# Optimization experiments

Measured on AMD Instinct MI355X. Metric: run time of the kernel, lower is better.

The kernel has to match this reference:

```python
import jax, jax.numpy as jnp
import numpy as np

N = 50000
E = 800000
IN_DIM, HID, OUT, DW = 128, 96, 40, 64
N_LBL = 10


def _deg_inv_sqrt(dst, n):
    # PyG gcn_norm: degree over target nodes of (A + I)
    deg = jax.ops.segment_sum(jnp.ones((dst.shape[0],), jnp.float32), dst, num_segments=n) + 1.0
    return jnp.where(deg > 0, 1.0 / jnp.sqrt(deg), 0.0)


def gcn_conv(h_in, W, b, src, dst, dinv):
    # GCNConv: out = D^-1/2 (A + I) D^-1/2 (X W) + b
    h = h_in @ W                                  # [N, F]
    norm = (dinv[src] * dinv[dst])[:, None]       # [E, 1]
    agg = jax.ops.segment_sum(h[src] * norm, dst, num_segments=h.shape[0])
    agg = agg + h * (dinv * dinv)[:, None]        # self-loop term
    return agg + b


def setup_inputs() -> dict:
    key = jax.random.key(0)
    ks = jax.random.split(key, 12)
    inp = {
        "x": jax.random.normal(ks[0], (N, IN_DIM), jnp.float32),
        "y": jax.random.uniform(ks[1], (N, OUT), jnp.float32),
        "edge_index": jax.random.randint(ks[2], (2, E), 0, N, jnp.int64 if jax.config.read("jax_enable_x64") else jnp.int32),
        "deep_walk_emb": jax.random.normal(ks[3], (N, DW), jnp.float32),
        # learned params
        "W_gcn1": jax.random.normal(ks[4], (IN_DIM, HID), jnp.float32) * (1.0 / np.sqrt(IN_DIM)),
        "b_gcn1": jnp.zeros((HID,), jnp.float32),
        "W_gcn2": jax.random.normal(ks[5], (HID, HID), jnp.float32) * (1.0 / np.sqrt(HID)),
        "b_gcn2": jnp.zeros((HID,), jnp.float32),
        "W_lbl": jax.random.normal(ks[6], (N_LBL, OUT, OUT), jnp.float32) * (1.0 / np.sqrt(OUT)),
        "b_lbl": jnp.zeros((N_LBL, OUT), jnp.float32),
        "W_fuse": jax.random.normal(ks[7], (HID + OUT + DW, OUT), jnp.float32) * (1.0 / np.sqrt(HID + OUT + DW)),
        "b_fuse": jnp.zeros((OUT,), jnp.float32),
    }
    return inp


def reference(x, y, edge_index, deep_walk_emb,
              W_gcn1, b_gcn1, W_gcn2, b_gcn2,
              W_lbl, b_lbl, W_fuse, b_fuse):
    src, dst = edge_index[0], edge_index[1]
    dinv = _deg_inv_sqrt(dst, x.shape[0])

    # feature propagation: 2 stacked GCNConv layers
    h = gcn_conv(x, W_gcn1, b_gcn1, src, dst, dinv)
    h = gcn_conv(h, W_gcn2, b_gcn2, src, dst, dinv)

    # label propagation: 10 stacked GCNConv layers via scan over stacked weights
    def step(carry, wb):
        W, b = wb
        return gcn_conv(carry, W, b, src, dst, dinv), None

    x_label, _ = jax.lax.scan(step, y, (W_lbl, b_lbl))

    fused = jnp.concatenate([h, x_label, deep_walk_emb], axis=1)  # [N, HID+OUT+DW]
    out = fused @ W_fuse + b_fuse
    return jax.nn.sigmoid(out)
```

## Files before the change

kernel.cpp:

```cpp
#include <hip/hip_runtime.h>
#include <hip/hip_bf16.h>
#include <math.h>

#define THREADS 256
typedef _Float16 h16;

__device__ __forceinline__ void ld8h(const h16* p, float* f) {
    union { uint4 u; h16 h[8]; } c;
    c.u = *(const uint4*)p;
#pragma unroll
    for (int j = 0; j < 8; ++j) f[j] = (float)c.h[j];
}

__global__ __launch_bounds__(256) void count_part_kernel(
    const int* __restrict__ dst, int* __restrict__ cnt, int E, int n)
{
    const int cls = blockIdx.x & 7;
    const int nb  = gridDim.x >> 3;
    const int sub = blockIdx.x >> 3;
    const int lo = (int)((long long)n * cls / 8);
    const int hi = (int)((long long)n * (cls + 1) / 8);
    const int stride = nb * 256;
    for (int e = sub * 256 + threadIdx.x; e < E; e += stride) {
        int d = dst[e];
        if (d >= lo && d < hi) atomicAdd(&cnt[d], 1);
    }
}

__global__ __launch_bounds__(256) void scatter_part_kernel(
    const int* __restrict__ src, const int* __restrict__ dst,
    int* __restrict__ cursor, int* __restrict__ col, int E, int n)
{
    const int cls = blockIdx.x & 7;
    const int nb  = gridDim.x >> 3;
    const int sub = blockIdx.x >> 3;
    const int lo = (int)((long long)n * cls / 8);
    const int hi = (int)((long long)n * (cls + 1) / 8);
    const int stride = nb * 256;
    for (int e = sub * 256 + threadIdx.x; e < E; e += stride) {
        int d = dst[e];
        if (d >= lo && d < hi) {
            int p = atomicAdd(&cursor[d], 1);
            col[p] = src[e];
        }
    }
}

__global__ __launch_bounds__(256) void scanp1_pre_kernel(
    const int* __restrict__ cnt, int* __restrict__ partial, int n, int NB,
    const float* __restrict__ Wl, const float* __restrict__ bl,
    const float* __restrict__ W2, const float* __restrict__ b1,
    const float* __restrict__ b2, const float* __restrict__ Wf,
    float* __restrict__ CM, float* __restrict__ betas,
    float* __restrict__ T, float* __restrict__ betaf1p, float* __restrict__ b2p)
{
    __shared__ __align__(16) float smem[5200];
    const int tid = threadIdx.x;
    const int bid = blockIdx.x;

    if (bid < NB) {
        int* red = (int*)smem;
        int base = bid * 1024 + tid * 4;
        int s = 0;
        if (base + 3 < n) {
            int4 v = *(const int4*)(cnt + base);
            s = v.x + v.y + v.z + v.w;
        } else {
            for (int k = 0; k < 4; k++) { int i = base + k; if (i < n) s += cnt[i]; }
        }
        red[tid] = s;
        __syncthreads();
        for (int off = 128; off > 0; off >>= 1) {
            if (tid < off) red[tid] += red[tid + off];
            __syncthreads();
        }
        if (tid == 0) partial[bid] = red[0];
        return;
    }

    if (bid == NB) {
        float* Ca  = smem;
        float* Cb  = smem + 1600;
        float* sWm = smem + 3200;
        float* bls = smem + 4800;
        for (int idx = tid; idx < 100; idx += 256)
            ((float4*)bls)[idx] = ((const float4*)bl)[idx];
        for (int idx = tid; idx < 400; idx += 256)
            ((float4*)Ca)[idx] = ((const float4*)(Wf + 3840))[idx];
        __syncthreads();
        if (tid < 40) {
            float s = 0.f;
#pragma unroll
            for (int k = 0; k < 40; ++k) s = fmaf(bls[360 + k], Ca[k * 40 + tid], s);
            betas[360 + tid] = s;
        }
        __syncthreads();
        float* cur = Ca;
        float* nxt = Cb;
        for (int m = 9; m >= 0; --m) {
            for (int idx = tid; idx < 400; idx += 256)
                ((float4*)sWm)[idx] = ((const float4*)(Wl + (size_t)m * 1600))[idx];
            __syncthreads();
            for (int sid = tid; sid < 400; sid += 256) {
                int i = sid / 10, jq = sid - (sid / 10) * 10;
                const float4* wr4 = (const float4*)&sWm[i * 40];
                const float4* c4 = (const float4*)cur;
                float4 a = make_float4(0.f, 0.f, 0.f, 0.f);
#pragma unroll
                for (int k4 = 0; k4 < 10; ++k4) {
                    float4 w = wr4[k4];
                    float4 c0 = c4[(k4 * 4 + 0) * 10 + jq];
                    float4 c1 = c4[(k4 * 4 + 1) * 10 + jq];
                    float4 c2 = c4[(k4 * 4 + 2) * 10 + jq];
                    float4 c3 = c4[(k4 * 4 + 3) * 10 + jq];
                    a.x = fmaf(w.x, c0.x, fmaf(w.y, c1.x, fmaf(w.z, c2.x, fmaf(w.w, c3.x, a.x))));
                    a.y = fmaf(w.x, c0.y, fmaf(w.y, c1.y, fmaf(w.z, c2.y, fmaf(w.w, c3.y, a.y))));
                    a.z = fmaf(w.x, c0.z, fmaf(w.y, c1.z, fmaf(w.z, c2.z, fmaf(w.w, c3.z, a.z))));
                    a.w = fmaf(w.x, c0.w, fmaf(w.y, c1.w, fmaf(w.z, c2.w, fmaf(w.w, c3.w, a.w))));
                }
                ((float4*)nxt)[sid] = a;
            }
            __syncthreads();
            if (m >= 1 && tid < 40) {
                float s = 0.f;
                const float* br = &bls[(m - 1) * 40];
#pragma unroll
                for (int k = 0; k < 40; ++k) s = fmaf(br[k], nxt[k * 40 + tid], s);
                betas[(size_t)(m - 1) * 40 + tid] = s;
            }
            float* t = cur; cur = nxt; nxt = t;
            __syncthreads();
        }
        for (int idx = tid; idx < 1600; idx += 256) CM[idx] = cur[idx];
        __syncthreads();

        float* sWf1 = smem;
        float* vq   = smem + 3840;
        for (int q2 = tid; q2 < 960; q2 += 256)
            ((float4*)sWf1)[q2] = ((const float4*)Wf)[q2];
        if (tid < 96) {
            float s = 0.f;
            for (int k = 0; k < 96; ++k) s = fmaf(b1[k], W2[(size_t)k * 96 + tid], s);
            vq[tid] = s;
        }
        __syncthreads();
        if (tid < 40) {
            float s1 = 0.f, s2 = 0.f;
            for (int q = 0; q < 96; ++q) {
                float w = sWf1[q * 40 + tid];
                s1 = fmaf(vq[q], w, s1);
                s2 = fmaf(b2[q], w, s2);
            }
            betaf1p[tid] = s1;
            b2p[tid] = s2;
        }
        return;
    }

    {
        int tb = bid - NB - 1;
        int idx = tb * 256 + tid;
        float* sWf1 = smem;
        for (int q2 = tid; q2 < 960; q2 += 256)
            ((float4*)sWf1)[q2] = ((const float4*)Wf)[q2];
        __syncthreads();
        int k = idx / 40, j = idx - (idx / 40) * 40;
        float s = 0.f;
#pragma unroll 8
        for (int q = 0; q < 96; ++q) s = fmaf(W2[(size_t)k * 96 + q], sWf1[q * 40 + j], s);
        T[idx] = s;
    }
}

template<int FIN, int FOUT, typename TX, typename TO, int DODINV>
__device__ __forceinline__ void gemm_body(
    const TX* __restrict__ X, const float* __restrict__ W,
    const float* __restrict__ dinv, TO* __restrict__ Y, int n,
    float* sX, float* sW, int bid, int tid)
{
    constexpr int KC = (FIN % 32 == 0) ? 32 : FIN;
    constexpr int NCHUNK = FIN / KC;
    constexpr int TN = (FOUT + 15) / 16;
    constexpr int BM = 64;
    constexpr int KP = KC + 4;

    const int tj = tid & 15;
    const int ti = tid >> 4;
    const int i0 = bid * BM;

    float acc[4][TN] = {};

    for (int c = 0; c < NCHUNK; ++c) {
        const int k0 = c * KC;
        __syncthreads();
        if constexpr (sizeof(TX) == 2) {
            constexpr int K8 = KC / 8;
            for (int v = tid; v < BM * K8; v += 256) {
                int r = v / K8, q = v - r * K8;
                int gi = i0 + r;
                float f[8] = {0.f, 0.f, 0.f, 0.f, 0.f, 0.f, 0.f, 0.f};
                if (gi < n) ld8h((const h16*)X + (size_t)gi * FIN + k0 + q * 8, f);
                float* p = &sX[r * KP + q * 8];
#pragma unroll
                for (int j = 0; j < 8; ++j) p[j] = f[j];
            }
        } else {
            constexpr int K4 = KC / 4;
            for (int v = tid; v < BM * K4; v += 256) {
                int r = v / K4, q = v - r * K4;
                int gi = i0 + r;
                float4 val = (gi < n) ? *(const float4*)((const float*)X + (size_t)gi * FIN + k0 + q * 4)
                                      : make_float4(0.f, 0.f, 0.f, 0.f);
                float* p = &sX[r * KP + q * 4];
                p[0] = val.x; p[1] = val.y; p[2] = val.z; p[3] = val.w;
            }
        }
        for (int v = tid; v < KC * FOUT; v += 256) {
            int kk = v / FOUT;
            int j = v - kk * FOUT;
            sW[j * KP + kk] = W[(size_t)(k0 + kk) * FOUT + j];
        }
        __syncthreads();
#pragma unroll
        for (int kk = 0; kk < KC; kk += 4) {
            float4 xv[4];
#pragma unroll
            for (int m = 0; m < 4; ++m)
                xv[m] = *(const float4*)&sX[(ti + 16 * m) * KP + kk];
#pragma unroll
            for (int u = 0; u < TN; ++u) {
                float4 wv = *(const float4*)&sW[(tj + 16 * u) * KP + kk];
#pragma unroll
                for (int m = 0; m < 4; ++m) {
                    acc[m][u] = fmaf(xv[m].x, wv.x, acc[m][u]);
                    acc[m][u] = fmaf(xv[m].y, wv.y, acc[m][u]);
                    acc[m][u] = fmaf(xv[m].z, wv.z, acc[m][u]);
                    acc[m][u] = fmaf(xv[m].w, wv.w, acc[m][u]);
                }
            }
        }
    }

#pragma unroll
    for (int m = 0; m < 4; ++m) {
        int gi = i0 + ti + 16 * m;
        if (gi >= n) continue;
        float dv = 1.f;
        if constexpr (DODINV) dv = dinv[gi];
#pragma unroll
        for (int u = 0; u < TN; ++u) {
            int j = tj + 16 * u;
            if (j < FOUT) Y[(size_t)gi * FOUT + j] = (TO)(acc[m][u] * dv);
        }
    }
}

template<int FIN, int FOUT, typename TX, typename TO, int DODINV>
__global__ __launch_bounds__(256) void gemm_kernel(
    const TX* __restrict__ X, const float* __restrict__ W,
    const float* __restrict__ dinv, TO* __restrict__ Y, int n)
{
    constexpr int KC = (FIN % 32 == 0) ? 32 : FIN;
    constexpr int KP = KC + 4;
    constexpr int TN = (FOUT + 15) / 16;
    __shared__ __align__(16) float smem[64 * KP + TN * 16 * KP];
    gemm_body<FIN, FOUT, TX, TO, DODINV>(X, W, dinv, Y, n, smem, smem + 64 * KP,
                                         blockIdx.x, threadIdx.x);
}

__global__ __launch_bounds__(256) void scanp2_wf_dw_kernel(
    int* __restrict__ partial, int* __restrict__ rowptr, int nb, int n,
    const float* __restrict__ W1, const float* __restrict__ T, float* __restrict__ WF,
    const float* __restrict__ dwe, const float* __restrict__ Wfbot, float* __restrict__ DW40)
{
    __shared__ __align__(16) float smem[4032];
    const int tid = threadIdx.x;
    const int bid = blockIdx.x;
    if (bid == 0) {
        int* sm = (int*)smem;
        int v = (tid < nb) ? partial[tid] : 0;
        sm[tid] = v;
        __syncthreads();
        int acc = v;
        for (int off = 1; off < 256; off <<= 1) {
            int t = (tid >= off) ? sm[tid - off] : 0;
            __syncthreads();
            acc += t;
            sm[tid] = acc;
            __syncthreads();
        }
        if (tid < nb) partial[tid] = acc - v;
        if (tid == 255) rowptr[n] = sm[255];
        return;
    }
    if (bid <= 20) {
        for (int idx = tid; idx < 960; idx += 256)
            ((float4*)smem)[idx] = ((const float4*)T)[idx];
        __syncthreads();
        int idx = (bid - 1) * 256 + tid;
        int i = idx / 40, j = idx - (idx / 40) * 40;
        float s = 0.f;
#pragma unroll 8
        for (int k = 0; k < 96; ++k) s = fmaf(W1[(size_t)i * 96 + k], smem[k * 40 + j], s);
        WF[idx] = s;
        return;
    }
    gemm_body<64, 40, float, float, 0>(dwe, Wfbot, nullptr, DW40, n,
                                       smem, smem + 2304, bid - 21, tid);
}

__global__ __launch_bounds__(256) void scan_p3(const int* __restrict__ cnt, const int* __restrict__ partial,
                                               int* __restrict__ rowptr, int* __restrict__ cursor,
                                               float* __restrict__ dinv, int n) {
    __shared__ int tsum[256];
    int tid = threadIdx.x;
    int base = blockIdx.x * 1024 + tid * 4;
    int v0 = 0, v1 = 0, v2 = 0, v3 = 0;
    if (base + 3 < n) {
        int4 t = *(const int4*)(cnt + base);
        v0 = t.x; v1 = t.y; v2 = t.z; v3 = t.w;
    } else {
        if (base + 0 < n) v0 = cnt[base + 0];
        if (base + 1 < n) v1 = cnt[base + 1];
        if (base + 2 < n) v2 = cnt[base + 2];
        if (base + 3 < n) v3 = cnt[base + 3];
    }
    int s = v0 + v1 + v2 + v3;
    tsum[tid] = s;
    __syncthreads();
    int acc = s;
    for (int off = 1; off < 256; off <<= 1) {
        int t = (tid >= off) ? tsum[tid - off] : 0;
        __syncthreads();
        acc += t;
        tsum[tid] = acc;
        __syncthreads();
    }
    int run = partial[blockIdx.x] + acc - s;
    int vv[4] = {v0, v1, v2, v3};
    for (int k = 0; k < 4; k++) {
        int i = base + k;
        if (i < n) {
            rowptr[i] = run; cursor[i] = run; run += vv[k];
            dinv[i] = rsqrtf((float)vv[k] + 1.0f);
        }
    }
}

template<int F, int MODE>
__device__ __forceinline__ void agg_body(
    const h16* __restrict__ hs, const int* __restrict__ rowptr,
    const int* __restrict__ col, const float* __restrict__ dinv,
    const float* __restrict__ bias, h16* __restrict__ out, int n,
    int bid, int tid,
    const float* __restrict__ extra32 = nullptr,
    const h16* __restrict__ f2 = nullptr,
    const float* __restrict__ bfp = nullptr,
    float* __restrict__ outf = nullptr)
{
    constexpr int F8 = F / 8;
    int gt = bid * 256 + tid;
    if (gt >= n * F8) return;
    int i = gt / F8;
    int f = gt - i * F8;
    int s = rowptr[i], e = rowptr[i + 1];
    const h16* base = hs + (size_t)f * 8;
    float acc[8];
    ld8h(hs + (size_t)i * F + f * 8, acc);
    int k = s;
    for (; k + 8 <= e; k += 8) {
        int c[8];
        union { uint4 u; h16 h[8]; } a[8];
#pragma unroll
        for (int q = 0; q < 8; ++q) c[q] = col[k + q];
#pragma unroll
        for (int q = 0; q < 8; ++q) a[q].u = *(const uint4*)(base + (size_t)c[q] * F);
#pragma unroll
        for (int j = 0; j < 8; ++j) {
            float t0 = ((float)a[0].h[j] + (float)a[1].h[j]) + ((float)a[2].h[j] + (float)a[3].h[j]);
            float t1 = ((float)a[4].h[j] + (float)a[5].h[j]) + ((float)a[6].h[j] + (float)a[7].h[j]);
            acc[j] += t0 + t1;
        }
    }
    for (; k + 4 <= e; k += 4) {
        int c0 = col[k], c1 = col[k + 1], c2 = col[k + 2], c3 = col[k + 3];
        union { uint4 u; h16 h[8]; } a0, a1, a2, a3;
        a0.u = *(const uint4*)(base + (size_t)c0 * F);
        a1.u = *(const uint4*)(base + (size_t)c1 * F);
        a2.u = *(const uint4*)(base + (size_t)c2 * F);
        a3.u = *(const uint4*)(base + (size_t)c3 * F);
#pragma unroll
        for (int j = 0; j < 8; ++j)
            acc[j] += ((float)a0.h[j] + (float)a1.h[j]) + ((float)a2.h[j] + (float)a3.h[j]);
    }
    for (; k < e; k++) {
        float v[8];
        ld8h(base + (size_t)col[k] * F, v);
#pragma unroll
        for (int j = 0; j < 8; ++j) acc[j] += v[j];
    }
    float dv = dinv[i];
    if constexpr (MODE == 3) {
        float fv[8];
        ld8h(f2 + (size_t)i * F + f * 8, fv);
        float r[8];
#pragma unroll
        for (int j = 0; j < 8; ++j) {
            float t = acc[j] * dv + bias[f * 8 + j] + fv[j] + bfp[f * 8 + j];
            r[j] = 1.f / (1.f + expf(-t));
        }
        float* po = outf + (size_t)i * F + f * 8;
        *(float4*)po       = make_float4(r[0], r[1], r[2], r[3]);
        *(float4*)(po + 4) = make_float4(r[4], r[5], r[6], r[7]);
    } else if constexpr (MODE == 2) {
        const float* pe = extra32 + (size_t)i * F + f * 8;
        float4 e0 = *(const float4*)pe;
        float4 e1 = *(const float4*)(pe + 4);
        float ex[8] = {e0.x, e0.y, e0.z, e0.w, e1.x, e1.y, e1.z, e1.w};
        union { uint4 u; h16 h[8]; } o;
#pragma unroll
        for (int j = 0; j < 8; ++j) o.h[j] = (h16)(acc[j] * dv + bias[f * 8 + j] + ex[j]);
        *(uint4*)(out + (size_t)i * F + f * 8) = o.u;
    } else {
        union { uint4 u; h16 h[8]; } o;
#pragma unroll
        for (int j = 0; j < 8; ++j) o.h[j] = (h16)((acc[j] * dv + bias[f * 8 + j]) * dv);
        *(uint4*)(out + (size_t)i * F + f * 8) = o.u;
    }
}

__global__ __launch_bounds__(256) void agg40_pre_kernel(
    const h16* __restrict__ hs, const int* __restrict__ rowptr,
    const int* __restrict__ col, const float* __restrict__ dinv,
    const float* __restrict__ bias, h16* __restrict__ out, int n) {
    agg_body<40, 1>(hs, rowptr, col, dinv, bias, out, n, blockIdx.x, threadIdx.x);
}

__global__ __launch_bounds__(256) void agg_hop1_kernel(
    const h16* __restrict__ hsA, const float* __restrict__ biasA, h16* __restrict__ outA,
    const h16* __restrict__ hsB, const float* __restrict__ biasB, h16* __restrict__ outB,
    const int* __restrict__ rowptr, const int* __restrict__ col,
    const float* __restrict__ dinv, int n, int nblkA)
{
    if (blockIdx.x < nblkA)
        agg_body<40, 1>(hsA, rowptr, col, dinv, biasA, outA, n, blockIdx.x, threadIdx.x);
    else
        agg_body<40, 1>(hsB, rowptr, col, dinv, biasB, outB, n, blockIdx.x - nblkA, threadIdx.x);
}

__global__ __launch_bounds__(256) void agg_hop2_kernel(
    const h16* __restrict__ hsA, const float* __restrict__ biasA, h16* __restrict__ outA,
    const h16* __restrict__ hsB, const float* __restrict__ biasB, h16* __restrict__ outB,
    const float* __restrict__ dw40,
    const int* __restrict__ rowptr, const int* __restrict__ col,
    const float* __restrict__ dinv, int n, int nblkA)
{
    if (blockIdx.x < nblkA)
        agg_body<40, 1>(hsA, rowptr, col, dinv, biasA, outA, n, blockIdx.x, threadIdx.x);
    else
        agg_body<40, 2>(hsB, rowptr, col, dinv, biasB, outB, n, blockIdx.x - nblkA, threadIdx.x, dw40);
}

__global__ __launch_bounds__(256) void agg_final_kernel(
    const h16* __restrict__ hs, const int* __restrict__ rowptr,
    const int* __restrict__ col, const float* __restrict__ dinv,
    const float* __restrict__ bias, const h16* __restrict__ f2,
    const float* __restrict__ bf, float* __restrict__ outf, int n)
{
    agg_body<40, 3>(hs, rowptr, col, dinv, bias, nullptr, n, blockIdx.x, threadIdx.x,
                    nullptr, f2, bf, outf);
}

extern "C" void kernel_launch(void* const* d_in, const int* in_sizes, int n_in,
                              void* d_out, int out_size, void* d_ws, size_t ws_size,
                              hipStream_t stream) {
    const float* x   = (const float*)d_in[0];
    const float* y   = (const float*)d_in[1];
    const int*   ei  = (const int*)d_in[2];
    const float* dwe = (const float*)d_in[3];
    const float* W1  = (const float*)d_in[4];
    const float* b1  = (const float*)d_in[5];
    const float* W2  = (const float*)d_in[6];
    const float* b2  = (const float*)d_in[7];
    const float* Wl  = (const float*)d_in[8];
    const float* bl  = (const float*)d_in[9];
    const float* Wf  = (const float*)d_in[10];
    const float* bf  = (const float*)d_in[11];
    float* out = (float*)d_out;

    const int n = in_sizes[0] / 128;
    const int E = in_sizes[2] / 2;
    const int* srcp = ei;
    const int* dstp = ei + E;

    char* ws = (char*)d_ws;
    size_t off = 0;
    auto alloc = [&](size_t bytes) -> void* {
        void* p = ws + off;
        off += bytes;
        off = (off + 255) & ~(size_t)255;
        return p;
    };

    int*   cnt     = (int*)alloc((size_t)n * 4);
    float* dinv    = (float*)alloc((size_t)n * 4);
    int*   rowptr  = (int*)alloc((size_t)(n + 1) * 4);
    int*   cursor  = (int*)alloc((size_t)n * 4);
    int*   partial = (int*)alloc(256 * 4);
    int*   col     = (int*)alloc((size_t)E * 4);
    h16*   Z0      = (h16*)alloc((size_t)n * 40 * 2);
    h16*   LA      = (h16*)alloc((size_t)n * 40 * 2);
    h16*   LB      = (h16*)alloc((size_t)n * 40 * 2);
    h16*   F0      = (h16*)alloc((size_t)n * 40 * 2);
    h16*   FB      = (h16*)alloc((size_t)n * 40 * 2);
    h16*   F2      = (h16*)alloc((size_t)n * 40 * 2);
    float* DW40    = (float*)alloc((size_t)n * 40 * 4);
    float* CM      = (float*)alloc(1600 * 4);
    float* betas   = (float*)alloc(10 * 40 * 4);
    float* T       = (float*)alloc(96 * 40 * 4);
    float* WF      = (float*)alloc(128 * 40 * 4);
    float* betaf1p = (float*)alloc(40 * 4);
    float* b2p     = (float*)alloc(40 * 4);
    (void)ws_size;

    const int NB      = (n + 1023) / 1024;
    const int gb_gm   = (n + 63) / 64;
    const int gb_a40  = (n * 5 + THREADS - 1) / THREADS;
    const int PART_BLOCKS = 2048;

    hipMemsetAsync(cnt, 0, (size_t)n * 4, stream);
    count_part_kernel<<<PART_BLOCKS, THREADS, 0, stream>>>(dstp, cnt, E, n);
    scanp1_pre_kernel<<<NB + 16, THREADS, 0, stream>>>(
        cnt, partial, n, NB, Wl, bl, W2, b1, b2, Wf, CM, betas, T, betaf1p, b2p);
    scanp2_wf_dw_kernel<<<21 + gb_gm, THREADS, 0, stream>>>(
        partial, rowptr, NB, n, W1, T, WF, dwe, Wf + 136 * 40, DW40);
    scan_p3<<<NB, THREADS, 0, stream>>>(cnt, partial, rowptr, cursor, dinv, n);
    scatter_part_kernel<<<PART_BLOCKS, THREADS, 0, stream>>>(srcp, dstp, cursor, col, E, n);

    gemm_kernel<40, 40, float, h16, 1><<<gb_gm, THREADS, 0, stream>>>(y, CM, dinv, Z0, n);
    gemm_kernel<128, 40, float, h16, 1><<<gb_gm, THREADS, 0, stream>>>(x, WF, dinv, F0, n);

    agg_hop1_kernel<<<2 * gb_a40, THREADS, 0, stream>>>(
        Z0, betas + 0, LA, F0, betaf1p, FB, rowptr, col, dinv, n, gb_a40);
    agg_hop2_kernel<<<2 * gb_a40, THREADS, 0, stream>>>(
        LA, betas + 40, LB, FB, b2p, F2, DW40, rowptr, col, dinv, n, gb_a40);

    const h16* cur = LB;
    for (int m = 3; m <= 9; m++) {
        h16* nxt = (m & 1) ? LA : LB;
        agg40_pre_kernel<<<gb_a40, THREADS, 0, stream>>>(
            cur, rowptr, col, dinv, betas + (size_t)(m - 1) * 40, nxt, n);
        cur = nxt;
    }

    agg_final_kernel<<<gb_a40, THREADS, 0, stream>>>(
        cur, rowptr, col, dinv, betas + 9 * 40, F2, bf, out, n);
}
```

Baseline: 345.8 us.

## Process aggregation rows in degree-sorted order via bucketed permutation

Builds a 64-bucket in-degree histogram, scans it into bucket offsets, and scatters node ids into a permutation array grouped by degree. All aggregation kernels then map thread slots to nodes through this permutation. The aim is to cut wavefront divergence from threads in one wave having very different edge counts. In exchange, output writes and self-term reads become scattered, nodes within a bucket land in atomic-dependent order, and setup gains extra atomics and an indirection load.

Measured after the change: 500.7 us. 44.8% more time.

```diff
diff --git a/kernel.cpp b/kernel.cpp
--- a/kernel.cpp
+++ b/kernel.cpp
@@ -29,10 +29,23 @@
 
 __global__ __launch_bounds__(256) void scatter_part_kernel(
     const int* __restrict__ src, const int* __restrict__ dst,
-    int* __restrict__ cursor, int* __restrict__ col, int E, int n)
-{
+    int* __restrict__ cursor, int* __restrict__ col, int E, int n, int PB,
+    const int* __restrict__ cnt, int* __restrict__ bucketCur, int* __restrict__ perm)
+{
+    if (blockIdx.x >= PB) {
+        int base = (blockIdx.x - PB) * 1024 + threadIdx.x * 4;
+        for (int k = 0; k < 4; ++k) {
+            int i = base + k;
+            if (i < n) {
+                int d = cnt[i]; if (d > 63) d = 63;
+                int pos = atomicAdd(&bucketCur[d], 1);
+                perm[pos] = i;
+            }
+        }
+        return;
+    }
     const int cls = blockIdx.x & 7;
-    const int nb  = gridDim.x >> 3;
+    const int nb  = PB >> 3;
     const int sub = blockIdx.x >> 3;
     const int lo = (int)((long long)n * cls / 8);
     const int hi = (int)((long long)n * (cls + 1) / 8);
@@ -52,7 +65,8 @@
     const float* __restrict__ W2, const float* __restrict__ b1,
     const float* __restrict__ b2, const float* __restrict__ Wf,
     float* __restrict__ CM, float* __restrict__ betas,
-    float* __restrict__ T, float* __restrict__ betaf1p, float* __restrict__ b2p)
+    float* __restrict__ T, float* __restrict__ betaf1p, float* __restrict__ b2p,
+    int* __restrict__ hist)
 {
     __shared__ __align__(16) float smem[5200];
     const int tid = threadIdx.x;
@@ -157,7 +171,7 @@
         return;
     }
 
-    {
+    if (bid < NB + 16) {
         int tb = bid - NB - 1;
         int idx = tb * 256 + tid;
         float* sWf1 = smem;
@@ -169,6 +183,24 @@
 #pragma unroll 8
         for (int q = 0; q < 96; ++q) s = fmaf(W2[(size_t)k * 96 + q], sWf1[q * 40 + j], s);
         T[idx] = s;
+        return;
+    }
+
+    {
+        int* lh = (int*)smem;
+        for (int b = tid; b < 64; b += 256) lh[b] = 0;
+        __syncthreads();
+        int base = (bid - NB - 16) * 1024 + tid * 4;
+        for (int k = 0; k < 4; ++k) {
+            int i = base + k;
+            if (i < n) {
+                int d = cnt[i]; if (d > 63) d = 63;
+                atomicAdd(&lh[d], 1);
+            }
+        }
+        __syncthreads();
+        for (int b = tid; b < 64; b += 256)
+            if (lh[b] > 0) atomicAdd(&hist[b], lh[b]);
     }
 }
 
@@ -311,9 +343,17 @@
 
 __global__ __launch_bounds__(256) void scan_p3(const int* __restrict__ cnt, const int* __restrict__ partial,
                                                int* __restrict__ rowptr, int* __restrict__ cursor,
-                                               float* __restrict__ dinv, int n) {
+                                               float* __restrict__ dinv, int n, int NB,
+                                               const int* __restrict__ hist, int* __restrict__ bucketCur) {
     __shared__ int tsum[256];
     int tid = threadIdx.x;
+    if (blockIdx.x == NB) {
+        if (tid == 0) {
+            int run = 0;
+            for (int b = 0; b < 64; ++b) { bucketCur[b] = run; run += hist[b]; }
+        }
+        return;
+    }
     int base = blockIdx.x * 1024 + tid * 4;
     int v0 = 0, v1 = 0, v2 = 0, v3 = 0;
     if (base + 3 < n) {
@@ -352,7 +392,7 @@
     const h16* __restrict__ hs, const int* __restrict__ rowptr,
     const int* __restrict__ col, const float* __restrict__ dinv,
     const float* __restrict__ bias, h16* __restrict__ out, int n,
-    int bid, int tid,
+    int bid, int tid, const int* __restrict__ perm,
     const float* __restrict__ extra32 = nullptr,
     const h16* __restrict__ f2 = nullptr,
     const float* __restrict__ bfp = nullptr,
@@ -361,8 +401,9 @@
     constexpr int F8 = F / 8;
     int gt = bid * 256 + tid;
     if (gt >= n * F8) return;
-    int i = gt / F8;
-    int f = gt - i * F8;
+    int slot = gt / F8;
+    int f = gt - slot * F8;
+    int i = perm[slot];
     int s = rowptr[i], e = rowptr[i + 1];
     const h16* base = hs + (size_t)f * 8;
     float acc[8];
@@ -432,20 +473,21 @@
 __global__ __launch_bounds__(256) void agg40_pre_kernel(
     const h16* __restrict__ hs, const int* __restrict__ rowptr,
     const int* __restrict__ col, const float* __restrict__ dinv,
-    const float* __restrict__ bias, h16* __restrict__ out, int n) {
-    agg_body<40, 1>(hs, rowptr, col, dinv, bias, out, n, blockIdx.x, threadIdx.x);
+    const float* __restrict__ bias, h16* __restrict__ out, int n,
+    const int* __restrict__ perm) {
+    agg_body<40, 1>(hs, rowptr, col, dinv, bias, out, n, blockIdx.x, threadIdx.x, perm);
 }
 
 __global__ __launch_bounds__(256) void agg_hop1_kernel(
     const h16* __restrict__ hsA, const float* __restrict__ biasA, h16* __restrict__ outA,
     const h16* __restrict__ hsB, const float* __restrict__ biasB, h16* __restrict__ outB,
     const int* __restrict__ rowptr, const int* __restrict__ col,
-    const float* __restrict__ dinv, int n, int nblkA)
+    const float* __restrict__ dinv, int n, int nblkA, const int* __restrict__ perm)
 {
     if (blockIdx.x < nblkA)
-        agg_body<40, 1>(hsA, rowptr, col, dinv, biasA, outA, n, blockIdx.x, threadIdx.x);
+        agg_body<40, 1>(hsA, rowptr, col, dinv, biasA, outA, n, blockIdx.x, threadIdx.x, perm);
     else
-        agg_body<40, 1>(hsB, rowptr, col, dinv, biasB, outB, n, blockIdx.x - nblkA, threadIdx.x);
+        agg_body<40, 1>(hsB, rowptr, col, dinv, biasB, outB, n, blockIdx.x - nblkA, threadIdx.x, perm);
 }
 
 __global__ __launch_bounds__(256) void agg_hop2_kernel(
@@ -453,22 +495,23 @@
     const h16* __restrict__ hsB, const float* __restrict__ biasB, h16* __restrict__ outB,
     const float* __restrict__ dw40,
     const int* __restrict__ rowptr, const int* __restrict__ col,
-    const float* __restrict__ dinv, int n, int nblkA)
+    const float* __restrict__ dinv, int n, int nblkA, const int* __restrict__ perm)
 {
     if (blockIdx.x < nblkA)
-        agg_body<40, 1>(hsA, rowptr, col, dinv, biasA, outA, n, blockIdx.x, threadIdx.x);
+        agg_body<40, 1>(hsA, rowptr, col, dinv, biasA, outA, n, blockIdx.x, threadIdx.x, perm);
     else
-        agg_body<40, 2>(hsB, rowptr, col, dinv, biasB, outB, n, blockIdx.x - nblkA, threadIdx.x, dw40);
+        agg_body<40, 2>(hsB, rowptr, col, dinv, biasB, outB, n, blockIdx.x - nblkA, threadIdx.x, perm, dw40);
 }
 
 __global__ __launch_bounds__(256) void agg_final_kernel(
     const h16* __restrict__ hs, const int* __restrict__ rowptr,
     const int* __restrict__ col, const float* __restrict__ dinv,
     const float* __restrict__ bias, const h16* __restrict__ f2,
-    const float* __restrict__ bf, float* __restrict__ outf, int n)
+    const float* __restrict__ bf, float* __restrict__ outf, int n,
+    const int* __restrict__ perm)
 {
     agg_body<40, 3>(hs, rowptr, col, dinv, bias, nullptr, n, blockIdx.x, threadIdx.x,
-                    nullptr, f2, bf, outf);
+                    perm, nullptr, f2, bf, outf);
 }
 
 extern "C" void kernel_launch(void* const* d_in, const int* in_sizes, int n_in,
@@ -503,11 +546,14 @@
     };
 
     int*   cnt     = (int*)alloc((size_t)n * 4);
+    int*   hist    = (int*)alloc(64 * 4);
+    int*   bucketCur = (int*)alloc(64 * 4);
     float* dinv    = (float*)alloc((size_t)n * 4);
     int*   rowptr  = (int*)alloc((size_t)(n + 1) * 4);
     int*   cursor  = (int*)alloc((size_t)n * 4);
     int*   partial = (int*)alloc(256 * 4);
     int*   col     = (int*)alloc((size_t)E * 4);
+    int*   perm    = (int*)alloc((size_t)n * 4);
     h16*   Z0      = (h16*)alloc((size_t)n * 40 * 2);
     h16*   LA      = (h16*)alloc((size_t)n * 40 * 2);
     h16*   LB      = (h16*)alloc((size_t)n * 40 * 2);
@@ -528,31 +574,32 @@
     const int gb_a40  = (n * 5 + THREADS - 1) / THREADS;
     const int PART_BLOCKS = 2048;
 
-    hipMemsetAsync(cnt, 0, (size_t)n * 4, stream);
+    hipMemsetAsync(cnt, 0, (size_t)((char*)dinv - (char*)cnt), stream);
     count_part_kernel<<<PART_BLOCKS, THREADS, 0, stream>>>(dstp, cnt, E, n);
-    scanp1_pre_kernel<<<NB + 16, THREADS, 0, stream>>>(
-        cnt, partial, n, NB, Wl, bl, W2, b1, b2, Wf, CM, betas, T, betaf1p, b2p);
+    scanp1_pre_kernel<<<NB + 16 + NB, THREADS, 0, stream>>>(
+        cnt, partial, n, NB, Wl, bl, W2, b1, b2, Wf, CM, betas, T, betaf1p, b2p, hist);
     scanp2_wf_dw_kernel<<<21 + gb_gm, THREADS, 0, stream>>>(
         partial, rowptr, NB, n, W1, T, WF, dwe, Wf + 136 * 40, DW40);
-    scan_p3<<<NB, THREADS, 0, stream>>>(cnt, partial, rowptr, cursor, dinv, n);
-    scatter_part_kernel<<<PART_BLOCKS, THREADS, 0, stream>>>(srcp, dstp, cursor, col, E, n);
+    scan_p3<<<NB + 1, THREADS, 0, stream>>>(cnt, partial, rowptr, cursor, dinv, n, NB, hist, bucketCur);
+    scatter_part_kernel<<<PART_BLOCKS + NB, THREADS, 0, stream>>>(
+        srcp, dstp, cursor, col, E, n, PART_BLOCKS, cnt, bucketCur, perm);
 
     gemm_kernel<40, 40, float, h16, 1><<<gb_gm, THREADS, 0, stream>>>(y, CM, dinv, Z0, n);
     gemm_kernel<128, 40, float, h16, 1><<<gb_gm, THREADS, 0, stream>>>(x, WF, dinv, F0, n);
 
     agg_hop1_kernel<<<2 * gb_a40, THREADS, 0, stream>>>(
-        Z0, betas + 0, LA, F0, betaf1p, FB, rowptr, col, dinv, n, gb_a40);
+        Z0, betas + 0, LA, F0, betaf1p, FB, rowptr, col, dinv, n, gb_a40, perm);
     agg_hop2_kernel<<<2 * gb_a40, THREADS, 0, stream>>>(
-        LA, betas + 40, LB, FB, b2p, F2, DW40, rowptr, col, dinv, n, gb_a40);
+        LA, betas + 40, LB, FB, b2p, F2, DW40, rowptr, col, dinv, n, gb_a40, perm);
 
     const h16* cur = LB;
     for (int m = 3; m <= 9; m++) {
         h16* nxt = (m & 1) ? LA : LB;
         agg40_pre_kernel<<<gb_a40, THREADS, 0, stream>>>(
-            cur, rowptr, col, dinv, betas + (size_t)(m - 1) * 40, nxt, n);
+            cur, rowptr, col, dinv, betas + (size_t)(m - 1) * 40, nxt, n, perm);
         cur = nxt;
     }
 
     agg_final_kernel<<<gb_a40, THREADS, 0, stream>>>(
-        cur, rowptr, col, dinv, betas + 9 * 40, F2, bf, out, n);
-}
+        cur, rowptr, col, dinv, betas + 9 * 40, F2, bf, out, n, perm);
+}
```
